# Kernel optimization log

Measured on AMD Instinct MI355X. Metric: run time of the kernel, lower is better.

The kernel has to match this reference:

```python
import jax, jax.numpy as jnp
import numpy as np

EPS = 1e-8
M_MARGIN = 0.5  # circle-loss margin m


def _l2norm(x):
    # torch.cosine_similarity clamps the norm product at eps; clamping each norm is equivalent in effect for randn data
    return x / jnp.maximum(jnp.linalg.norm(x, axis=-1, keepdims=True), EPS)


def setup_inputs() -> dict:
    key = jax.random.key(0)
    k1, k2, k3, k4 = jax.random.split(key, 4)
    N, D = 8192, 1024
    return {
        "text_embeddings": jax.random.normal(k1, (N, D), dtype=jnp.float32),
        "text_pos_embeddings": jax.random.normal(k2, (N, D), dtype=jnp.float32),
        "text_neg_embeddings": jax.random.normal(k3, (N, D), dtype=jnp.float32),
        "text_neg_index": jax.random.randint(k4, (N,), 0, N, dtype=jnp.int64 if jax.config.jax_enable_x64 else jnp.int32),
    }


def reference(text_embeddings, text_pos_embeddings, text_neg_embeddings, text_neg_index):
    # use_all_pair=False, mixcse=-1 branch of RetriContrastLoss.forward
    q = _l2norm(text_embeddings)        # [N, D]
    p = _l2norm(text_pos_embeddings)    # [N, D]
    n = _l2norm(text_neg_embeddings)    # [M, D]

    # normalize-then-GEMM == cosine_similarity(unsqueeze(1), unsqueeze(0))
    sim_neg = jnp.einsum("nd,md->nm", q, n)       # [N, M] query-vs-neg cosines
    sim_pos = jnp.sum(q * p, axis=-1)             # [N]    query-vs-pos diagonal cosines
    # NOTE: temperature is never applied in this branch (faithful to source)

    m = M_MARGIN
    # negatives: an = clamp_min(detach(s) + (1+m), 0); s' = an * (s - delta_n), delta_n = -(1-m)
    an = jnp.maximum(jax.lax.stop_gradient(sim_neg) + (1.0 + m), 0.0)
    s_neg = an * (sim_neg + (1.0 - m))
    # positives: ap = clamp_min(-detach(s) + (1+m), 0); s' = -ap * (s - delta_p), delta_p = 1-m
    ap = jnp.maximum(-jax.lax.stop_gradient(sim_pos) + (1.0 + m), 0.0)
    s_pos = -ap * (sim_pos - (1.0 - m))

    # source flattens via boolean mask then logsumexp over dim=0 -> global logsumexp
    lse_neg = jax.scipy.special.logsumexp(s_neg.reshape(-1))
    lse_pos = jax.scipy.special.logsumexp(s_pos)
    return jax.nn.softplus(lse_neg + lse_pos)
```

## Files before the change

### kernel.cpp

```cpp
#include <hip/hip_runtime.h>
#include <hip/hip_bf16.h>
#include <hip/hip_fp8.h>

#define D_K 1024
#define TILE 128
#define BKB 128

typedef int intx8 __attribute__((ext_vector_type(8)));
typedef float floatx4 __attribute__((ext_vector_type(4)));

__device__ __forceinline__ unsigned char f2fp8(float x) {
    __hip_fp8_e4m3 v(x);
    return v.__x;
}

__device__ __forceinline__ void gl_lds16(const void* g, void* l) {
    __builtin_amdgcn_global_load_lds(
        (const __attribute__((address_space(1))) unsigned int*)g,
        (__attribute__((address_space(3))) unsigned int*)l,
        16, 0, 0);
}

__device__ __forceinline__ intx8 ld_frag(const unsigned char* rowbase, int quad, int e) {
    const int4 lo = *(const int4*)(rowbase + (((2 * quad) ^ e) * 16));
    const int4 hi = *(const int4*)(rowbase + (((2 * quad + 1) ^ e) * 16));
    intx8 v;
    v[0] = lo.x; v[1] = lo.y; v[2] = lo.z; v[3] = lo.w;
    v[4] = hi.x; v[5] = hi.y; v[6] = hi.z; v[7] = hi.w;
    return v;
}

__global__ __launch_bounds__(256)
void prep_kernel(const float* __restrict__ q, const float* __restrict__ p,
                 const float* __restrict__ ng,
                 unsigned char* __restrict__ qn, unsigned char* __restrict__ nn,
                 float* __restrict__ posp) {
    const int row = blockIdx.x;
    const int t = threadIdx.x;
    const size_t base = (size_t)row * D_K;

    float4 qa = ((const float4*)(q + base))[t];
    float4 pa = ((const float4*)(p + base))[t];
    float4 na = ((const float4*)(ng + base))[t];

    float4 v;
    v.x = qa.x*qa.x + qa.y*qa.y + qa.z*qa.z + qa.w*qa.w;
    v.y = pa.x*pa.x + pa.y*pa.y + pa.z*pa.z + pa.w*pa.w;
    v.z = qa.x*pa.x + qa.y*pa.y + qa.z*pa.z + qa.w*pa.w;
    v.w = na.x*na.x + na.y*na.y + na.z*na.z + na.w*na.w;

    for (int off = 32; off > 0; off >>= 1) {
        v.x += __shfl_down(v.x, off);
        v.y += __shfl_down(v.y, off);
        v.z += __shfl_down(v.z, off);
        v.w += __shfl_down(v.w, off);
    }
    __shared__ float4 red[4];
    const int wid = t >> 6, lane = t & 63;
    if (lane == 0) red[wid] = v;
    __syncthreads();
    float4 tot;
    tot.x = red[0].x + red[1].x + red[2].x + red[3].x;
    tot.y = red[0].y + red[1].y + red[2].y + red[3].y;
    tot.z = red[0].z + red[1].z + red[2].z + red[3].z;
    tot.w = red[0].w + red[1].w + red[2].w + red[3].w;

    const float rq = 1.0f / fmaxf(sqrtf(tot.x), 1e-8f);
    const float rn = 1.0f / fmaxf(sqrtf(tot.w), 1e-8f);

    uchar4 pk;
    pk.x = f2fp8(qa.x * rq); pk.y = f2fp8(qa.y * rq);
    pk.z = f2fp8(qa.z * rq); pk.w = f2fp8(qa.w * rq);
    *(uchar4*)(qn + base + 4 * (size_t)t) = pk;
    pk.x = f2fp8(na.x * rn); pk.y = f2fp8(na.y * rn);
    pk.z = f2fp8(na.z * rn); pk.w = f2fp8(na.w * rn);
    *(uchar4*)(nn + base + 4 * (size_t)t) = pk;

    if (t == 0) {
        const float rp = 1.0f / fmaxf(sqrtf(tot.y), 1e-8f);
        const float sim = tot.z * rq * rp;
        const float ap = fmaxf(1.5f - sim, 0.0f);
        const float sp = -ap * (sim - 0.5f);
        posp[row] = __expf(sp - 4.0f);
    }
}

__global__ __launch_bounds__(256, 2)
void gemm_lse_fp8(const unsigned char* __restrict__ A,
                  const unsigned char* __restrict__ B,
                  float* __restrict__ negp) {
    __shared__ unsigned char As[TILE * BKB];
    __shared__ unsigned char Bs[TILE * BKB];

    const int tid = threadIdx.x;
    const int wid = tid >> 6;
    const int lane = tid & 63;
    const int tile_m = blockIdx.y * TILE;
    const int tile_n = blockIdx.x * TILE;

    const int wave_m = (wid & 1) * 64;
    const int wave_n = (wid >> 1) * 64;
    const int quad = lane >> 4;
    const int r = lane & 15;
    const int e = r & 7;

    floatx4 acc[4][4] = {};

    int lds_off[4];
    size_t src_off[4];
#pragma unroll
    for (int s = 0; s < 4; s++) {
        const int cc = s * 256 + tid;
        const int row = cc >> 3, slot = cc & 7;
        lds_off[s] = cc * 16;
        src_off[s] = (size_t)row * D_K + (size_t)((slot ^ (row & 7)) * 16);
    }
    const unsigned char* Ab = A + (size_t)tile_m * D_K;
    const unsigned char* Bb = B + (size_t)tile_n * D_K;

    for (int k0 = 0; k0 < D_K; k0 += BKB) {
#pragma unroll
        for (int s = 0; s < 4; s++) {
            gl_lds16(Ab + src_off[s] + k0, &As[lds_off[s]]);
            gl_lds16(Bb + src_off[s] + k0, &Bs[lds_off[s]]);
        }
        __syncthreads();

        intx8 a[4], b[4];
#pragma unroll
        for (int i = 0; i < 4; i++)
            a[i] = ld_frag(&As[(wave_m + i * 16 + r) * BKB], quad, e);
#pragma unroll
        for (int j = 0; j < 4; j++)
            b[j] = ld_frag(&Bs[(wave_n + j * 16 + r) * BKB], quad, e);

#pragma unroll
        for (int i = 0; i < 4; i++)
#pragma unroll
            for (int j = 0; j < 4; j++)
                acc[i][j] = __builtin_amdgcn_mfma_scale_f32_16x16x128_f8f6f4(
                    a[i], b[j], acc[i][j],
                    0, 0,
                    0, 0x7f7f7f7f,
                    0, 0x7f7f7f7f);

        __syncthreads();
    }

    float lsum = 0.0f;
#pragma unroll
    for (int i = 0; i < 4; i++)
#pragma unroll
        for (int j = 0; j < 4; j++)
#pragma unroll
            for (int el = 0; el < 4; el++) {
                const float s = acc[i][j][el];
                const float an = fmaxf(s + 1.5f, 0.0f);
                const float sn = an * (s + 0.5f);
                lsum += __expf(sn - 4.0f);
            }
    for (int off = 32; off > 0; off >>= 1) lsum += __shfl_down(lsum, off);
    __shared__ float red[4];
    if (lane == 0) red[wid] = lsum;
    __syncthreads();
    if (tid == 0)
        negp[blockIdx.y * gridDim.x + blockIdx.x] = red[0] + red[1] + red[2] + red[3];
}

__global__ __launch_bounds__(256)
void finalize_kernel(const float* __restrict__ negp, int n_neg,
                     const float* __restrict__ posp, int n_pos,
                     float* __restrict__ out) {
    double sn = 0.0, sp = 0.0;
    for (int i = threadIdx.x; i < n_neg; i += 256) sn += (double)negp[i];
    for (int i = threadIdx.x; i < n_pos; i += 256) sp += (double)posp[i];
    for (int off = 32; off > 0; off >>= 1) {
        sn += __shfl_down(sn, off);
        sp += __shfl_down(sp, off);
    }
    __shared__ double rn[4], rp[4];
    const int wid = threadIdx.x >> 6, lane = threadIdx.x & 63;
    if (lane == 0) { rn[wid] = sn; rp[wid] = sp; }
    __syncthreads();
    if (threadIdx.x == 0) {
        const double NS = rn[0] + rn[1] + rn[2] + rn[3];
        const double PS = rp[0] + rp[1] + rp[2] + rp[3];
        const double x = (4.0 + log(NS)) + (4.0 + log(PS));
        const double spl = (x > 30.0) ? x : log1p(exp(x));
        out[0] = (float)spl;
    }
}

extern "C" void kernel_launch(void* const* d_in, const int* in_sizes, int n_in,
                              void* d_out, int out_size, void* d_ws, size_t ws_size,
                              hipStream_t stream) {
    const float* q = (const float*)d_in[0];
    const float* p = (const float*)d_in[1];
    const float* ng = (const float*)d_in[2];

    const int N = in_sizes[3];
    const int D = in_sizes[0] / N;
    const int M = in_sizes[2] / D;

    char* ws = (char*)d_ws;
    unsigned char* qn = (unsigned char*)ws;
    unsigned char* nn = (unsigned char*)(ws + (size_t)N * D);
    float* negp = (float*)(ws + (size_t)(N + M) * D);
    const int n_neg = (N / TILE) * (M / TILE);
    float* posp = negp + n_neg;

    prep_kernel<<<N, 256, 0, stream>>>(q, p, ng, qn, nn, posp);
    gemm_lse_fp8<<<dim3(M / TILE, N / TILE), 256, 0, stream>>>(qn, nn, negp);
    finalize_kernel<<<1, 256, 0, stream>>>(negp, n_neg, posp, N, (float*)d_out);
}
```

Baseline: 199.8 us.

## Enlarge GEMM tile to 256x128 with 8 waves, one-wave-per-row prep

The GEMM block grows from 128x128 with 4 waves to 256x128 with 8 waves. The B tile is now shared across twice as many rows, which reduces global/LDS traffic per MFMA, and launch bounds move to (512,4). The prep kernel now handles one row per wave, so the block-level LDS reduction and barrier become wave shuffles. The finalize kernel uses 1024 threads. Risks are higher LDS use per block (48KB) and register pressure that could limit occupancy.

```diff
diff --git a/kernel.cpp b/kernel.cpp
--- a/kernel.cpp
+++ b/kernel.cpp
@@ -3,7 +3,8 @@
 #include <hip/hip_fp8.h>
 
 #define D_K 1024
-#define TILE 128
+#define TM 256
+#define TN 128
 #define BKB 128
 
 typedef int intx8 __attribute__((ext_vector_type(8)));
@@ -35,94 +36,91 @@
                  const float* __restrict__ ng,
                  unsigned char* __restrict__ qn, unsigned char* __restrict__ nn,
                  float* __restrict__ posp) {
-    const int row = blockIdx.x;
-    const int t = threadIdx.x;
+    const int wid = threadIdx.x >> 6, lane = threadIdx.x & 63;
+    const int row = blockIdx.x * 4 + wid;
     const size_t base = (size_t)row * D_K;
-
-    float4 qa = ((const float4*)(q + base))[t];
-    float4 pa = ((const float4*)(p + base))[t];
-    float4 na = ((const float4*)(ng + base))[t];
-
-    float4 v;
-    v.x = qa.x*qa.x + qa.y*qa.y + qa.z*qa.z + qa.w*qa.w;
-    v.y = pa.x*pa.x + pa.y*pa.y + pa.z*pa.z + pa.w*pa.w;
-    v.z = qa.x*pa.x + qa.y*pa.y + qa.z*pa.z + qa.w*pa.w;
-    v.w = na.x*na.x + na.y*na.y + na.z*na.z + na.w*na.w;
-
-    for (int off = 32; off > 0; off >>= 1) {
-        v.x += __shfl_down(v.x, off);
-        v.y += __shfl_down(v.y, off);
-        v.z += __shfl_down(v.z, off);
-        v.w += __shfl_down(v.w, off);
-    }
-    __shared__ float4 red[4];
-    const int wid = t >> 6, lane = t & 63;
-    if (lane == 0) red[wid] = v;
-    __syncthreads();
-    float4 tot;
-    tot.x = red[0].x + red[1].x + red[2].x + red[3].x;
-    tot.y = red[0].y + red[1].y + red[2].y + red[3].y;
-    tot.z = red[0].z + red[1].z + red[2].z + red[3].z;
-    tot.w = red[0].w + red[1].w + red[2].w + red[3].w;
-
-    const float rq = 1.0f / fmaxf(sqrtf(tot.x), 1e-8f);
-    const float rn = 1.0f / fmaxf(sqrtf(tot.w), 1e-8f);
-
-    uchar4 pk;
-    pk.x = f2fp8(qa.x * rq); pk.y = f2fp8(qa.y * rq);
-    pk.z = f2fp8(qa.z * rq); pk.w = f2fp8(qa.w * rq);
-    *(uchar4*)(qn + base + 4 * (size_t)t) = pk;
-    pk.x = f2fp8(na.x * rn); pk.y = f2fp8(na.y * rn);
-    pk.z = f2fp8(na.z * rn); pk.w = f2fp8(na.w * rn);
-    *(uchar4*)(nn + base + 4 * (size_t)t) = pk;
-
-    if (t == 0) {
-        const float rp = 1.0f / fmaxf(sqrtf(tot.y), 1e-8f);
-        const float sim = tot.z * rq * rp;
+    const float4* q4 = (const float4*)(q + base);
+    const float4* p4 = (const float4*)(p + base);
+    const float4* n4 = (const float4*)(ng + base);
+
+    float4 qa[4], na[4];
+    float qq = 0.f, pp = 0.f, qp = 0.f, nn2 = 0.f;
+#pragma unroll
+    for (int j = 0; j < 4; j++) {
+        qa[j] = q4[j * 64 + lane];
+        float4 pa = p4[j * 64 + lane];
+        na[j] = n4[j * 64 + lane];
+        qq += qa[j].x*qa[j].x + qa[j].y*qa[j].y + qa[j].z*qa[j].z + qa[j].w*qa[j].w;
+        pp += pa.x*pa.x + pa.y*pa.y + pa.z*pa.z + pa.w*pa.w;
+        qp += qa[j].x*pa.x + qa[j].y*pa.y + qa[j].z*pa.z + qa[j].w*pa.w;
+        nn2 += na[j].x*na[j].x + na[j].y*na[j].y + na[j].z*na[j].z + na[j].w*na[j].w;
+    }
+#pragma unroll
+    for (int off = 1; off < 64; off <<= 1) {
+        qq += __shfl_xor(qq, off);
+        pp += __shfl_xor(pp, off);
+        qp += __shfl_xor(qp, off);
+        nn2 += __shfl_xor(nn2, off);
+    }
+    const float rq = 1.0f / fmaxf(sqrtf(qq), 1e-8f);
+    const float rn = 1.0f / fmaxf(sqrtf(nn2), 1e-8f);
+
+#pragma unroll
+    for (int j = 0; j < 4; j++) {
+        uchar4 pk;
+        pk.x = f2fp8(qa[j].x * rq); pk.y = f2fp8(qa[j].y * rq);
+        pk.z = f2fp8(qa[j].z * rq); pk.w = f2fp8(qa[j].w * rq);
+        ((uchar4*)(qn + base))[j * 64 + lane] = pk;
+        pk.x = f2fp8(na[j].x * rn); pk.y = f2fp8(na[j].y * rn);
+        pk.z = f2fp8(na[j].z * rn); pk.w = f2fp8(na[j].w * rn);
+        ((uchar4*)(nn + base))[j * 64 + lane] = pk;
+    }
+
+    if (lane == 0) {
+        const float rp = 1.0f / fmaxf(sqrtf(pp), 1e-8f);
+        const float sim = qp * rq * rp;
         const float ap = fmaxf(1.5f - sim, 0.0f);
         const float sp = -ap * (sim - 0.5f);
         posp[row] = __expf(sp - 4.0f);
     }
 }
 
-__global__ __launch_bounds__(256, 2)
+__global__ __launch_bounds__(512, 4)
 void gemm_lse_fp8(const unsigned char* __restrict__ A,
                   const unsigned char* __restrict__ B,
                   float* __restrict__ negp) {
-    __shared__ unsigned char As[TILE * BKB];
-    __shared__ unsigned char Bs[TILE * BKB];
+    __shared__ unsigned char As[TM * BKB];
+    __shared__ unsigned char Bs[TN * BKB];
 
     const int tid = threadIdx.x;
     const int wid = tid >> 6;
     const int lane = tid & 63;
-    const int tile_m = blockIdx.y * TILE;
-    const int tile_n = blockIdx.x * TILE;
-
-    const int wave_m = (wid & 1) * 64;
-    const int wave_n = (wid >> 1) * 64;
+    const int tile_m = blockIdx.y * TM;
+    const int tile_n = blockIdx.x * TN;
+
+    const int wave_m = (wid & 3) * 64;
+    const int wave_n = (wid >> 2) * 64;
     const int quad = lane >> 4;
     const int r = lane & 15;
     const int e = r & 7;
 
     floatx4 acc[4][4] = {};
 
-    int lds_off[4];
-    size_t src_off[4];
-#pragma unroll
-    for (int s = 0; s < 4; s++) {
-        const int cc = s * 256 + tid;
-        const int row = cc >> 3, slot = cc & 7;
-        lds_off[s] = cc * 16;
-        src_off[s] = (size_t)row * D_K + (size_t)((slot ^ (row & 7)) * 16);
-    }
     const unsigned char* Ab = A + (size_t)tile_m * D_K;
     const unsigned char* Bb = B + (size_t)tile_n * D_K;
 
     for (int k0 = 0; k0 < D_K; k0 += BKB) {
 #pragma unroll
         for (int s = 0; s < 4; s++) {
-            gl_lds16(Ab + src_off[s] + k0, &As[lds_off[s]]);
-            gl_lds16(Bb + src_off[s] + k0, &Bs[lds_off[s]]);
+            const int cc = s * 512 + tid;
+            const int row = cc >> 3, slot = cc & 7;
+            gl_lds16(Ab + (size_t)row * D_K + k0 + ((slot ^ (row & 7)) * 16), &As[cc * 16]);
+        }
+#pragma unroll
+        for (int s = 0; s < 2; s++) {
+            const int cc = s * 512 + tid;
+            const int row = cc >> 3, slot = cc & 7;
+            gl_lds16(Bb + (size_t)row * D_K + k0 + ((slot ^ (row & 7)) * 16), &Bs[cc * 16]);
         }
         __syncthreads();
 
@@ -160,31 +158,36 @@
                 lsum += __expf(sn - 4.0f);
             }
     for (int off = 32; off > 0; off >>= 1) lsum += __shfl_down(lsum, off);
-    __shared__ float red[4];
+    __shared__ float red[8];
     if (lane == 0) red[wid] = lsum;
     __syncthreads();
-    if (tid == 0)
-        negp[blockIdx.y * gridDim.x + blockIdx.x] = red[0] + red[1] + red[2] + red[3];
-}
-
-__global__ __launch_bounds__(256)
+    if (tid == 0) {
+        float t = 0.f;
+#pragma unroll
+        for (int w = 0; w < 8; w++) t += red[w];
+        negp[blockIdx.y * gridDim.x + blockIdx.x] = t;
+    }
+}
+
+__global__ __launch_bounds__(1024)
 void finalize_kernel(const float* __restrict__ negp, int n_neg,
                      const float* __restrict__ posp, int n_pos,
                      float* __restrict__ out) {
     double sn = 0.0, sp = 0.0;
-    for (int i = threadIdx.x; i < n_neg; i += 256) sn += (double)negp[i];
-    for (int i = threadIdx.x; i < n_pos; i += 256) sp += (double)posp[i];
+    for (int i = threadIdx.x; i < n_neg; i += 1024) sn += (double)negp[i];
+    for (int i = threadIdx.x; i < n_pos; i += 1024) sp += (double)posp[i];
     for (int off = 32; off > 0; off >>= 1) {
         sn += __shfl_down(sn, off);
         sp += __shfl_down(sp, off);
     }
-    __shared__ double rn[4], rp[4];
+    __shared__ double rn[16], rp[16];
     const int wid = threadIdx.x >> 6, lane = threadIdx.x & 63;
     if (lane == 0) { rn[wid] = sn; rp[wid] = sp; }
     __syncthreads();
     if (threadIdx.x == 0) {
-        const double NS = rn[0] + rn[1] + rn[2] + rn[3];
-        const double PS = rp[0] + rp[1] + rp[2] + rp[3];
+        double NS = 0.0, PS = 0.0;
+#pragma unroll
+        for (int w = 0; w < 16; w++) { NS += rn[w]; PS += rp[w]; }
         const double x = (4.0 + log(NS)) + (4.0 + log(PS));
         const double spl = (x > 30.0) ? x : log1p(exp(x));
         out[0] = (float)spl;
@@ -206,10 +209,10 @@
     unsigned char* qn = (unsigned char*)ws;
     unsigned char* nn = (unsigned char*)(ws + (size_t)N * D);
     float* negp = (float*)(ws + (size_t)(N + M) * D);
-    const int n_neg = (N / TILE) * (M / TILE);
+    const int n_neg = (M / TN) * (N / TM);
     float* posp = negp + n_neg;
 
-    prep_kernel<<<N, 256, 0, stream>>>(q, p, ng, qn, nn, posp);
-    gemm_lse_fp8<<<dim3(M / TILE, N / TILE), 256, 0, stream>>>(qn, nn, negp);
-    finalize_kernel<<<1, 256, 0, stream>>>(negp, n_neg, posp, N, (float*)d_out);
-}
+    prep_kernel<<<N / 4, 256, 0, stream>>>(q, p, ng, qn, nn, posp);
+    gemm_lse_fp8<<<dim3(M / TN, N / TM), 512, 0, stream>>>(qn, nn, negp);
+    finalize_kernel<<<1, 1024, 0, stream>>>(negp, n_neg, posp, N, (float*)d_out);
+}
```

After: 369.5 us. +85.0%, slower.
